# Kernel tuning notes

Measured on AMD Instinct MI355X. Metric: run time of the kernel, lower is better.

## Reference

```python
import jax, jax.numpy as jnp
import numpy as np

B_, S, D = 4, 1024, 1024
MULT, HEAD_DIM, M, K, CFAC = 4, 64, 16, 2, 1.25
H = MULT * D


def _layer_norm(x, g, b, eps=1e-5):
    mu = jnp.mean(x, axis=-1, keepdims=True)
    var = jnp.var(x, axis=-1, keepdims=True)
    return (x - mu) * jax.lax.rsqrt(var + eps) * g + b


def setup_inputs() -> dict:
    key = jax.random.key(0)
    ks = jax.random.split(key, 10)
    sc = 0.02
    return {
        "x": jax.random.normal(ks[0], (B_, S, D), jnp.float32),
        "ln1_g": jnp.ones((D,), jnp.float32), "ln1_b": jnp.zeros((D,), jnp.float32),
        "qkv_w": jax.random.normal(ks[1], (3 * D, D), jnp.float32) * sc,
        "qkv_b": jnp.zeros((3 * D,), jnp.float32),
        "attn_in_w": jax.random.normal(ks[2], (3 * D, D), jnp.float32) * sc,
        "attn_in_b": jnp.zeros((3 * D,), jnp.float32),
        "attn_out_w": jax.random.normal(ks[3], (D, D), jnp.float32) * sc,
        "attn_out_b": jnp.zeros((D,), jnp.float32),
        "ln2_g": jnp.ones((D,), jnp.float32), "ln2_b": jnp.zeros((D,), jnp.float32),
        "r_w1": jax.random.normal(ks[4], (H, D), jnp.float32) * sc,
        "r_b1": jnp.zeros((H,), jnp.float32),
        "r_w2": jax.random.normal(ks[5], (M, H), jnp.float32) * sc,
        "r_b2": jnp.zeros((M,), jnp.float32),
        "mlp1": jax.random.normal(ks[6], (M, D, H), jnp.float32) / np.float32(np.sqrt(D)),
        "mlp2": jax.random.normal(ks[7], (M, H, D), jnp.float32) / np.float32(np.sqrt(H)),
    }


def reference(x, ln1_g, ln1_b, qkv_w, qkv_b, attn_in_w, attn_in_b,
              attn_out_w, attn_out_b, ln2_g, ln2_b, r_w1, r_b1, r_w2, r_b2,
              mlp1, mlp2):
    b, s, d = x.shape
    nh, hd = d // HEAD_DIM, HEAD_DIM

    # ---- attention block ----
    resid = x
    xn = _layer_norm(x, ln1_g, ln1_b)
    qkv = xn @ qkv_w.T + qkv_b              # [b,s,3d]
    q0, k0, v0 = jnp.split(qkv, 3, axis=-1)
    # nn.MultiheadAttention applies its own in/out projections on top
    wq, wk, wv = jnp.split(attn_in_w, 3, axis=0)
    bq, bk, bv = jnp.split(attn_in_b, 3, axis=0)
    q = (q0 @ wq.T + bq).reshape(b, s, nh, hd).transpose(0, 2, 1, 3)
    k = (k0 @ wk.T + bk).reshape(b, s, nh, hd).transpose(0, 2, 1, 3)
    v = (v0 @ wv.T + bv).reshape(b, s, nh, hd).transpose(0, 2, 1, 3)
    scores = jnp.einsum('bhqd,bhkd->bhqk', q, k) / np.float32(np.sqrt(hd))
    causal = jnp.triu(jnp.full((s, s), -jnp.inf, jnp.float32), k=1)
    attn = jax.nn.softmax(scores + causal, axis=-1)
    ao = jnp.einsum('bhqk,bhkd->bhqd', attn, v).transpose(0, 2, 1, 3).reshape(b, s, d)
    x1 = resid + (ao @ attn_out_w.T + attn_out_b)

    # ---- MoE MLP block ----
    resid2 = x1
    xn2 = _layer_norm(x1, ln2_g, ln2_b)
    B = b * s
    cap = int(B * CFAC * K // M)
    xf = xn2.reshape(B, d)
    # router
    logits = jax.nn.gelu(xf @ r_w1.T + r_b1, approximate=False) @ r_w2.T + r_b2  # [B,M]
    vals, inds = jax.lax.top_k(logits, K)
    probs = jax.nn.softmax(vals, axis=-1).reshape(-1)     # [B*K]
    indsf = inds.reshape(-1)                              # [B*K]
    # cumsum-based position within each expert's capacity buffer
    one_hot = jax.nn.one_hot(indsf, M, dtype=jnp.int32)
    counts = jnp.cumsum(one_hot, axis=0)
    pos = counts[jnp.arange(B * K), indsf] - 1
    keep = pos < cap
    flat_idx = indsf * cap + pos
    safe_idx = jnp.where(keep, flat_idx, M * cap)         # OOB index -> dropped
    src = jnp.repeat(xf, K, axis=0)                       # [B*K, d]
    expert_in = jnp.zeros((M * cap, d), xf.dtype).at[safe_idx].set(src, mode='drop')
    expert_in = expert_in.reshape(M, cap, d)
    # grouped GEMM experts
    mid = jax.nn.gelu(jnp.einsum('mcd,mdh->mch', expert_in, mlp1), approximate=False)
    eout = jnp.einsum('mch,mhd->mcd', mid, mlp2).reshape(M * cap, d)
    # combine
    g = eout[jnp.where(keep, flat_idx, 0)] * (probs * keep)[:, None]
    token_idx = jnp.repeat(jnp.arange(B), K)
    combined = jax.ops.segment_sum(g, token_idx, num_segments=B)
    has_kept = jax.ops.segment_sum(keep.astype(jnp.int32), token_idx, num_segments=B) > 0
    moe_out = jnp.where(has_kept[:, None], combined, xf)
    out = resid2 + moe_out.reshape(b, s, d)
    return out, logits.reshape(b, s, M)
```

## Files before the change

kernel.cpp:

```cpp
#include <hip/hip_runtime.h>
#include <math.h>

#define NTOK   4096
#define DIM    1024
#define H3     3072
#define HMLP   4096
#define NEXP   16
#define CAP    640
#define HCHUNK 1024
#define LSCALE 2048.0f
#define INV_LSCALE (1.0f / 2048.0f)

typedef _Float16 half8 __attribute__((ext_vector_type(8)));
typedef __attribute__((ext_vector_type(4))) float floatx4;
typedef __attribute__((ext_vector_type(8))) ushort us8;

#define F_QKV_HI   ((size_t)0)
#define F_QKV_LO   ((size_t)6291456)
#define F_XN_HI    ((size_t)12582912)
#define F_XN_LO    ((size_t)14680064)
#define F_H1       ((size_t)0)
#define F_EOUT     ((size_t)0)
#define F_Q16_HI   ((size_t)16777216)
#define F_K16_HI   ((size_t)18874368)
#define F_V16_HI   ((size_t)20971520)
#define F_Q16_LO   ((size_t)23068672)
#define F_K16_LO   ((size_t)25165824)
#define F_V16_LO   ((size_t)27262976)
#define F_VT_HI    ((size_t)12582912)
#define F_VT_LO    ((size_t)14680064)
#define F_AO_HI    ((size_t)29360128)
#define F_AO_LO    ((size_t)31457280)
#define F_XF_HI    ((size_t)33554432)
#define F_XF_LO    ((size_t)35651584)
#define F_WQKV_HI  ((size_t)37748736)
#define F_WQKV_LO  ((size_t)39321600)
#define F_WAIN_HI  ((size_t)40894464)
#define F_WAIN_LO  ((size_t)42467328)
#define F_WAOUT_HI ((size_t)44040192)
#define F_WAOUT_LO ((size_t)44564480)
#define F_WR1_HI   ((size_t)45088768)
#define F_WR1_LO   ((size_t)47185920)
#define F_EXPIN    ((size_t)16777216)
#define F_MLP1T    ((size_t)22020096)
#define F_MID      ((size_t)30408704)
#define F_MLP2T    ((size_t)35651584)
#define F_X1       ((size_t)49283072)
#define F_XF       ((size_t)53477376)
#define F_PROBS    ((size_t)57671680)
#define F_INDS     ((size_t)57679872)
#define F_KEEP     ((size_t)57688064)
#define F_FLAT     ((size_t)57696256)

__device__ __forceinline__ ushort f2h(float f) {
    _Float16 h = (_Float16)f;
    union { _Float16 h; ushort u; } c; c.h = h; return c.u;
}
__device__ __forceinline__ float h2f(ushort u) {
    union { ushort u; _Float16 h; } c; c.u = u; return (float)c.h;
}
__device__ __forceinline__ float gelu_exact(float x) {
    return 0.5f * x * (1.0f + erff(x * 0.7071067811865475f));
}

__device__ __forceinline__ void gl16(const void* g, void* l) {
    __builtin_amdgcn_global_load_lds(
        (const __attribute__((address_space(1))) void*)g,
        (__attribute__((address_space(3))) void*)l, 16, 0, 0);
}

__global__ __launch_bounds__(256) void split_f32(const float* __restrict__ x,
                                                 ushort* __restrict__ hi,
                                                 ushort* __restrict__ lo, int n4) {
    int i = blockIdx.x * 256 + threadIdx.x;
    if (i >= n4) return;
    float4 v = ((const float4*)x)[i];
    float vv[4] = {v.x, v.y, v.z, v.w};
    ushort h[4], l[4];
#pragma unroll
    for (int e = 0; e < 4; e++) {
        h[e] = f2h(vv[e]);
        l[e] = f2h((vv[e] - h2f(h[e])) * LSCALE);
    }
    ((ushort4*)hi)[i] = make_ushort4(h[0], h[1], h[2], h[3]);
    ((ushort4*)lo)[i] = make_ushort4(l[0], l[1], l[2], l[3]);
}

__global__ __launch_bounds__(256) void ln_kernel(const float* __restrict__ x,
                                                 const float* __restrict__ g,
                                                 const float* __restrict__ b,
                                                 float* __restrict__ yf,
                                                 ushort* __restrict__ yhi,
                                                 ushort* __restrict__ ylo) {
    __shared__ float red0[4], red1[4], bc[2];
    const size_t t = blockIdx.x;
    const float* row = x + t * DIM;
    float v[4];
    float s = 0.f, s2 = 0.f;
#pragma unroll
    for (int i = 0; i < 4; i++) {
        float vv = row[threadIdx.x + i * 256];
        v[i] = vv; s += vv; s2 += vv * vv;
    }
#pragma unroll
    for (int off = 32; off > 0; off >>= 1) {
        s  += __shfl_down(s, off);
        s2 += __shfl_down(s2, off);
    }
    const int lane = threadIdx.x & 63, wid = threadIdx.x >> 6;
    if (lane == 0) { red0[wid] = s; red1[wid] = s2; }
    __syncthreads();
    if (threadIdx.x == 0) {
        float S = red0[0] + red0[1] + red0[2] + red0[3];
        float S2 = red1[0] + red1[1] + red1[2] + red1[3];
        float mean = S * (1.0f / DIM);
        float var = S2 * (1.0f / DIM) - mean * mean;
        bc[0] = mean; bc[1] = rsqrtf(var + 1e-5f);
    }
    __syncthreads();
    const float mean = bc[0], r = bc[1];
#pragma unroll
    for (int i = 0; i < 4; i++) {
        int idx = threadIdx.x + i * 256;
        float val = (v[i] - mean) * r * g[idx] + b[idx];
        size_t o = t * DIM + idx;
        if (yf) yf[o] = val;
        if (yhi) {
            ushort h = f2h(val);
            yhi[o] = h;
            if (ylo) ylo[o] = f2h((val - h2f(h)) * LSCALE);
        }
    }
}

template<bool SPLIT>
__global__ __launch_bounds__(256) void gemm_ht(
    const ushort* __restrict__ Ahi, const ushort* __restrict__ Alo, int lda, long long sA,
    const ushort* __restrict__ Bhi, const ushort* __restrict__ Blo, int ldb, long long sB,
    const float* __restrict__ bias, long long sBias,
    const float* __restrict__ resid, int ldr,
    float* __restrict__ outf, ushort* __restrict__ outhi, ushort* __restrict__ outlo,
    int ldc, long long sC, int Kdim, int act, int accum) {
    __shared__ ushort sAh[128][32];
    __shared__ ushort sBh[128][32];
    __shared__ ushort sAl[SPLIT ? 128 : 1][32];
    __shared__ ushort sBl[SPLIT ? 128 : 1][32];
    const int z = blockIdx.z;
    Ahi += (size_t)z * sA; Bhi += (size_t)z * sB;
    if constexpr (SPLIT) { Alo += (size_t)z * sA; Blo += (size_t)z * sB; }
    if (bias) bias += (size_t)z * sBias;
    if (outf) outf += (size_t)z * sC;
    if (outhi) outhi += (size_t)z * sC;
    if (outlo) outlo += (size_t)z * sC;

    const int tid = threadIdx.x;
    const int row0 = blockIdx.y * 128, col0 = blockIdx.x * 128;
    const int lane = tid & 63;
    const int m = lane & 15, half = lane >> 4;
    const int w = tid >> 6;
    const int ar0 = (w >> 1) * 64, bc0 = (w & 1) * 64;

    const int srow = w * 32 + (lane >> 2);
    const int ssw  = (((lane >> 3) & 3) ^ (lane & 3)) * 8;
    const int rsw8 = ((((m >> 1) & 3) ^ half)) * 8;

    floatx4 acc[4][4];
    floatx4 acc2[SPLIT ? 4 : 1][SPLIT ? 4 : 1];
#pragma unroll
    for (int i = 0; i < 4; i++)
#pragma unroll
        for (int j = 0; j < 4; j++) acc[i][j] = (floatx4){0.f, 0.f, 0.f, 0.f};
    if constexpr (SPLIT) {
#pragma unroll
        for (int i = 0; i < 4; i++)
#pragma unroll
            for (int j = 0; j < 4; j++) acc2[i][j] = (floatx4){0.f, 0.f, 0.f, 0.f};
    }

    for (int k0 = 0; k0 < Kdim; k0 += 32) {
        __syncthreads();
        {
            const ushort* gA = Ahi + (size_t)(row0 + srow) * lda + k0 + ssw;
            const ushort* gB = Bhi + (size_t)(col0 + srow) * ldb + k0 + ssw;
            gl16(gA,                      &sAh[w * 32][0]);
            gl16(gA + (size_t)16 * lda,   &sAh[w * 32 + 16][0]);
            gl16(gB,                      &sBh[w * 32][0]);
            gl16(gB + (size_t)16 * ldb,   &sBh[w * 32 + 16][0]);
            if constexpr (SPLIT) {
                const ushort* gAl = Alo + (size_t)(row0 + srow) * lda + k0 + ssw;
                const ushort* gBl = Blo + (size_t)(col0 + srow) * ldb + k0 + ssw;
                gl16(gAl,                    &sAl[w * 32][0]);
                gl16(gAl + (size_t)16 * lda, &sAl[w * 32 + 16][0]);
                gl16(gBl,                    &sBl[w * 32][0]);
                gl16(gBl + (size_t)16 * ldb, &sBl[w * 32 + 16][0]);
            }
        }
        __syncthreads();
        half8 fa[4], fb[4], fal[4], fbl[4];
#pragma unroll
        for (int i = 0; i < 4; i++) fa[i] = *(const half8*)&sAh[ar0 + i * 16 + m][rsw8];
#pragma unroll
        for (int j = 0; j < 4; j++) fb[j] = *(const half8*)&sBh[bc0 + j * 16 + m][rsw8];
        if constexpr (SPLIT) {
#pragma unroll
            for (int i = 0; i < 4; i++) fal[i] = *(const half8*)&sAl[ar0 + i * 16 + m][rsw8];
#pragma unroll
            for (int j = 0; j < 4; j++) fbl[j] = *(const half8*)&sBl[bc0 + j * 16 + m][rsw8];
        }
#pragma unroll
        for (int i = 0; i < 4; i++)
#pragma unroll
            for (int j = 0; j < 4; j++) {
                acc[i][j] = __builtin_amdgcn_mfma_f32_16x16x32_f16(fa[i], fb[j], acc[i][j], 0, 0, 0);
                if constexpr (SPLIT) {
                    acc2[i][j] = __builtin_amdgcn_mfma_f32_16x16x32_f16(fa[i], fbl[j], acc2[i][j], 0, 0, 0);
                    acc2[i][j] = __builtin_amdgcn_mfma_f32_16x16x32_f16(fal[i], fb[j], acc2[i][j], 0, 0, 0);
                }
            }
    }
#pragma unroll
    for (int i = 0; i < 4; i++) {
#pragma unroll
        for (int j = 0; j < 4; j++) {
            const int col = col0 + bc0 + j * 16 + m;
            const float bv = bias ? bias[col] : 0.f;
#pragma unroll
            for (int r = 0; r < 4; r++) {
                const int row = row0 + ar0 + i * 16 + half * 4 + r;
                float v = acc[i][j][r];
                if constexpr (SPLIT) v += acc2[i][j][r] * INV_LSCALE;
                v += bv;
                if (resid) v += resid[(size_t)row * ldr + col];
                if (accum) v += outf[(size_t)row * ldc + col];
                if (act) v = gelu_exact(v);
                const size_t o = (size_t)row * ldc + col;
                if (outf) outf[o] = v;
                if (outhi) {
                    ushort h = f2h(v);
                    outhi[o] = h;
                    if (outlo) outlo[o] = f2h((v - h2f(h)) * LSCALE);
                }
            }
        }
    }
}

__global__ __launch_bounds__(256) void transpose_h(const float* __restrict__ in, long long sIn, int ldin,
                                                   ushort* __restrict__ out, long long sOut, int ldout) {
    __shared__ float t[32][33];
    const int z = blockIdx.z;
    in += (size_t)z * sIn; out += (size_t)z * sOut;
    const int cx = threadIdx.x & 31, ry = threadIdx.x >> 5;
    const int r0 = blockIdx.y * 32, c0 = blockIdx.x * 32;
#pragma unroll
    for (int rr = 0; rr < 4; rr++)
        t[ry + rr * 8][cx] = in[(size_t)(r0 + ry + rr * 8) * ldin + c0 + cx];
    __syncthreads();
#pragma unroll
    for (int rr = 0; rr < 4; rr++)
        out[(size_t)(c0 + ry + rr * 8) * ldout + r0 + cx] = f2h(t[cx][ry + rr * 8]);
}

__global__ __launch_bounds__(256) void vtrans_kernel(const ushort* __restrict__ vhi,
                                                     const ushort* __restrict__ vlo,
                                                     ushort* __restrict__ vthi,
                                                     ushort* __restrict__ vtlo) {
    __shared__ ushort th[32][72], tl[32][72];
    const int bh = blockIdx.y, b = bh >> 4, h = bh & 15;
    const int s0 = blockIdx.x * 32;
    const int t = threadIdx.x;
    {
        const int s = t >> 3, d0 = (t & 7) * 8;
        const size_t src = ((size_t)(b * 1024 + s0 + s)) * 1024 + h * 64 + d0;
        *(uint4*)&th[s][d0] = *(const uint4*)&vhi[src];
        *(uint4*)&tl[s][d0] = *(const uint4*)&vlo[src];
    }
    __syncthreads();
    {
        const int d = t >> 2, soff = (t & 3) * 8;
        us8 rh, rl;
#pragma unroll
        for (int e = 0; e < 8; e++) { rh[e] = th[soff + e][d]; rl[e] = tl[soff + e][d]; }
        const size_t dst = (size_t)bh * 65536 + (size_t)d * 1024 + s0 + soff;
        *(us8*)&vthi[dst] = rh;
        *(us8*)&vtlo[dst] = rl;
    }
}

__global__ __launch_bounds__(256, 2) void attn_mfma(
        const ushort* __restrict__ qh_, const ushort* __restrict__ ql_,
        const ushort* __restrict__ kh_, const ushort* __restrict__ kl_,
        const ushort* __restrict__ vth_, const ushort* __restrict__ vtl_,
        ushort* __restrict__ ao_hi, ushort* __restrict__ ao_lo) {
    __shared__ ushort plds[4][2][2048];
    const int bh = blockIdx.y;
    const int b = bh >> 4;
    const int qt = 7 - blockIdx.x;
    const int tid = threadIdx.x;
    const int w = tid >> 6, lane = tid & 63;
    const int m = lane & 15, hq = lane >> 4;
    const int wrow = qt * 128 + w * 32;
    const size_t cbase = ((size_t)b * 1024) * 1024 + (size_t)(bh & 15) * 64;
    const size_t vtbase = (size_t)bh * 65536;

    half8 qfh[2][2], qfl[2][2];
#pragma unroll
    for (int i = 0; i < 2; i++)
#pragma unroll
        for (int kk = 0; kk < 2; kk++) {
            const size_t o = cbase + (size_t)(wrow + i * 16 + m) * 1024 + kk * 32 + hq * 8;
            qfh[i][kk] = *(const half8*)&qh_[o];
            qfl[i][kk] = *(const half8*)&ql_[o];
        }

    floatx4 accO[2][4], accO2[2][4];
#pragma unroll
    for (int i = 0; i < 2; i++)
#pragma unroll
        for (int d = 0; d < 4; d++) {
            accO[i][d] = (floatx4){0.f, 0.f, 0.f, 0.f};
            accO2[i][d] = (floatx4){0.f, 0.f, 0.f, 0.f};
        }
    float mx[2][4], ls[2][4];
#pragma unroll
    for (int i = 0; i < 2; i++)
#pragma unroll
        for (int r = 0; r < 4; r++) { mx[i][r] = -3.0e38f; ls[i][r] = 0.f; }

    const int ntiles = (wrow + 31) / 64 + 1;
    for (int t = 0; t < ntiles; t++) {
        const int j0 = t * 64;
        floatx4 accS[2][4], accS2[2][4];
#pragma unroll
        for (int i = 0; i < 2; i++)
#pragma unroll
            for (int jf = 0; jf < 4; jf++) {
                accS[i][jf] = (floatx4){0.f, 0.f, 0.f, 0.f};
                accS2[i][jf] = (floatx4){0.f, 0.f, 0.f, 0.f};
            }
#pragma unroll
        for (int kk = 0; kk < 2; kk++) {
            half8 kfh[4], kfl[4];
#pragma unroll
            for (int jf = 0; jf < 4; jf++) {
                const size_t o = cbase + (size_t)(j0 + jf * 16 + m) * 1024 + kk * 32 + hq * 8;
                kfh[jf] = *(const half8*)&kh_[o];
                kfl[jf] = *(const half8*)&kl_[o];
            }
#pragma unroll
            for (int i = 0; i < 2; i++)
#pragma unroll
                for (int jf = 0; jf < 4; jf++) {
                    accS[i][jf] = __builtin_amdgcn_mfma_f32_16x16x32_f16(qfh[i][kk], kfh[jf], accS[i][jf], 0, 0, 0);
                    accS2[i][jf] = __builtin_amdgcn_mfma_f32_16x16x32_f16(qfh[i][kk], kfl[jf], accS2[i][jf], 0, 0, 0);
                    accS2[i][jf] = __builtin_amdgcn_mfma_f32_16x16x32_f16(qfl[i][kk], kfh[jf], accS2[i][jf], 0, 0, 0);
                }
        }
        const bool diag = (j0 + 63 > wrow);
        float p[2][4][4];
#pragma unroll
        for (int i = 0; i < 2; i++)
#pragma unroll
            for (int jf = 0; jf < 4; jf++)
#pragma unroll
                for (int r = 0; r < 4; r++) {
                    float s = (accS[i][jf][r] + accS2[i][jf][r] * INV_LSCALE) * 0.125f;
                    if (diag && (j0 + jf * 16 + m > wrow + i * 16 + hq * 4 + r)) s = -3.0e38f;
                    p[i][jf][r] = s;
                }
#pragma unroll
        for (int i = 0; i < 2; i++)
#pragma unroll
            for (int r = 0; r < 4; r++) {
                float tm = fmaxf(fmaxf(p[i][0][r], p[i][1][r]), fmaxf(p[i][2][r], p[i][3][r]));
#pragma unroll
                for (int off = 8; off > 0; off >>= 1) tm = fmaxf(tm, __shfl_xor(tm, off));
                const float mn = fmaxf(mx[i][r], tm);
                const float c = __expf(mx[i][r] - mn);
                mx[i][r] = mn;
                float rs = 0.f;
#pragma unroll
                for (int jf = 0; jf < 4; jf++) {
                    const float e = __expf(p[i][jf][r] - mn);
                    p[i][jf][r] = e;
                    rs += e;
                }
#pragma unroll
                for (int off = 8; off > 0; off >>= 1) rs += __shfl_xor(rs, off);
                ls[i][r] = ls[i][r] * c + rs;
#pragma unroll
                for (int d = 0; d < 4; d++) { accO[i][d][r] *= c; accO2[i][d][r] *= c; }
            }
#pragma unroll
        for (int i = 0; i < 2; i++)
#pragma unroll
            for (int jf = 0; jf < 4; jf++)
#pragma unroll
                for (int r = 0; r < 4; r++) {
                    const int row = i * 16 + hq * 4 + r;
                    const int idx = row * 64 + ((jf * 16 + m) ^ ((row & 7) << 3));
                    const float pv = p[i][jf][r];
                    const ushort hh = f2h(pv);
                    plds[w][0][idx] = hh;
                    plds[w][1][idx] = f2h((pv - h2f(hh)) * LSCALE);
                }
#pragma unroll
        for (int kk = 0; kk < 2; kk++) {
            half8 pfh[2], pfl[2], vfh[4], vfl[4];
#pragma unroll
            for (int i = 0; i < 2; i++) {
                const int row = i * 16 + m;
                const int idx = row * 64 + ((kk * 32 + hq * 8) ^ ((row & 7) << 3));
                pfh[i] = *(const half8*)&plds[w][0][idx];
                pfl[i] = *(const half8*)&plds[w][1][idx];
            }
#pragma unroll
            for (int d = 0; d < 4; d++) {
                const size_t o = vtbase + (size_t)(d * 16 + m) * 1024 + j0 + kk * 32 + hq * 8;
                vfh[d] = *(const half8*)&vth_[o];
                vfl[d] = *(const half8*)&vtl_[o];
            }
#pragma unroll
            for (int i = 0; i < 2; i++)
#pragma unroll
                for (int d = 0; d < 4; d++) {
                    accO[i][d] = __builtin_amdgcn_mfma_f32_16x16x32_f16(pfh[i], vfh[d], accO[i][d], 0, 0, 0);
                    accO2[i][d] = __builtin_amdgcn_mfma_f32_16x16x32_f16(pfh[i], vfl[d], accO2[i][d], 0, 0, 0);
                    accO2[i][d] = __builtin_amdgcn_mfma_f32_16x16x32_f16(pfl[i], vfh[d], accO2[i][d], 0, 0, 0);
                }
        }
    }
#pragma unroll
    for (int i = 0; i < 2; i++)
#pragma unroll
        for (int r = 0; r < 4; r++) {
            const float inv = 1.f / ls[i][r];
            const size_t rb = cbase + (size_t)(wrow + i * 16 + hq * 4 + r) * 1024;
#pragma unroll
            for (int d = 0; d < 4; d++) {
                const float v = (accO[i][d][r] + accO2[i][d][r] * INV_LSCALE) * inv;
                const ushort hh = f2h(v);
                const size_t o = rb + d * 16 + m;
                ao_hi[o] = hh;
                ao_lo[o] = f2h((v - h2f(hh)) * LSCALE);
            }
        }
}

__global__ __launch_bounds__(256) void router2_kernel(const float* __restrict__ h1,
                                                      const float* __restrict__ w2,
                                                      const float* __restrict__ b2,
                                                      float* __restrict__ logits_out,
                                                      float* __restrict__ probs,
                                                      int* __restrict__ inds) {
    __shared__ float red[16][4];
    __shared__ float lg[16];
    const int t = blockIdx.x;
    const float* hrow = h1 + (size_t)t * HMLP;
    float acc[16];
#pragma unroll
    for (int m = 0; m < 16; m++) acc[m] = 0.f;
    for (int i = 0; i < 16; i++) {
        int kk = threadIdx.x + i * 256;
        float hv = hrow[kk];
#pragma unroll
        for (int m = 0; m < 16; m++) acc[m] = fmaf(hv, w2[m * HMLP + kk], acc[m]);
    }
#pragma unroll
    for (int m = 0; m < 16; m++)
#pragma unroll
        for (int off = 32; off > 0; off >>= 1) acc[m] += __shfl_down(acc[m], off);
    const int lane = threadIdx.x & 63, wid = threadIdx.x >> 6;
    if (lane == 0) {
#pragma unroll
        for (int m = 0; m < 16; m++) red[m][wid] = acc[m];
    }
    __syncthreads();
    if (threadIdx.x < 16) {
        float v = red[threadIdx.x][0] + red[threadIdx.x][1] + red[threadIdx.x][2] + red[threadIdx.x][3]
                  + b2[threadIdx.x];
        lg[threadIdx.x] = v;
        logits_out[(size_t)t * 16 + threadIdx.x] = v;
    }
    __syncthreads();
    if (threadIdx.x == 0) {
        int i0 = 0; float v0 = lg[0];
        for (int m = 1; m < 16; m++) if (lg[m] > v0) { v0 = lg[m]; i0 = m; }
        int i1 = -1; float v1 = -3.4e38f;
        for (int m = 0; m < 16; m++) if (m != i0 && lg[m] > v1) { v1 = lg[m]; i1 = m; }
        float e1 = expf(v1 - v0);
        float den = 1.f + e1;
        inds[2 * t] = i0; inds[2 * t + 1] = i1;
        probs[2 * t] = 1.f / den; probs[2 * t + 1] = e1 / den;
    }
}

__global__ __launch_bounds__(256) void scan_kernel(const int* __restrict__ inds,
                                                   int* __restrict__ keep,
                                                   int* __restrict__ flat) {
    __shared__ int counts[256][16];
    const int t = threadIdx.x;
#pragma unroll
    for (int e = 0; e < 16; e++) counts[t][e] = 0;
    const int base = t * 32;
    for (int i = 0; i < 32; i++) counts[t][inds[base + i]]++;
    __syncthreads();
    if (t < 16) {
        int run = 0;
        for (int c = 0; c < 256; c++) { int tmp = counts[c][t]; counts[c][t] = run; run += tmp; }
    }
    __syncthreads();
    for (int i = 0; i < 32; i++) {
        int e = inds[base + i];
        int p = counts[t][e]++;
        keep[base + i] = (p < CAP) ? 1 : 0;
        flat[base + i] = e * CAP + p;
    }
}

__global__ __launch_bounds__(256) void scatter_kernel(const float* __restrict__ xf,
                                                      const int* __restrict__ keep,
                                                      const int* __restrict__ flat,
                                                      ushort* __restrict__ expert_in) {
    const int e = blockIdx.x;
    if (!keep[e]) return;
    const int token = e >> 1;
    const float* src = xf + (size_t)token * DIM;
    ushort* dst = expert_in + (size_t)flat[e] * DIM;
#pragma unroll
    for (int i = 0; i < 4; i++) dst[threadIdx.x + i * 256] = f2h(src[threadIdx.x + i * 256]);
}

__global__ __launch_bounds__(256) void combine_kernel(const float* __restrict__ x1,
                                                      const float* __restrict__ xf,
                                                      const float* __restrict__ eout,
                                                      const float* __restrict__ probs,
                                                      const int* __restrict__ keep,
                                                      const int* __restrict__ flat,
                                                      float* __restrict__ out) {
    const int t = blockIdx.x;
    const int k0 = keep[2 * t], k1 = keep[2 * t + 1];
    const float p0 = probs[2 * t], p1 = probs[2 * t + 1];
    const size_t f0 = (size_t)flat[2 * t] * DIM, f1 = (size_t)flat[2 * t + 1] * DIM;
    const bool has = (k0 || k1);
    const size_t base = (size_t)t * DIM;
#pragma unroll
    for (int i = 0; i < 4; i++) {
        const int idx = threadIdx.x + i * 256;
        float mo;
        if (has) {
            mo = 0.f;
            if (k0) mo += p0 * eout[f0 + idx];
            if (k1) mo += p1 * eout[f1 + idx];
        } else {
            mo = xf[base + idx];
        }
        out[base + idx] = x1[base + idx] + mo;
    }
}

extern "C" void kernel_launch(void* const* d_in, const int* in_sizes, int n_in,
                              void* d_out, int out_size, void* d_ws, size_t ws_size,
                              hipStream_t stream) {
    const float* x          = (const float*)d_in[0];
    const float* ln1_g      = (const float*)d_in[1];
    const float* ln1_b      = (const float*)d_in[2];
    const float* qkv_w      = (const float*)d_in[3];
    const float* qkv_b      = (const float*)d_in[4];
    const float* attn_in_w  = (const float*)d_in[5];
    const float* attn_in_b  = (const float*)d_in[6];
    const float* attn_out_w = (const float*)d_in[7];
    const float* attn_out_b = (const float*)d_in[8];
    const float* ln2_g      = (const float*)d_in[9];
    const float* ln2_b      = (const float*)d_in[10];
    const float* r_w1       = (const float*)d_in[11];
    const float* r_b1       = (const float*)d_in[12];
    const float* r_w2       = (const float*)d_in[13];
    const float* r_b2       = (const float*)d_in[14];
    const float* mlp1       = (const float*)d_in[15];
    const float* mlp2       = (const float*)d_in[16];

    float* ws = (float*)d_ws;
    ushort* qkv_hi   = (ushort*)(ws + F_QKV_HI);
    ushort* qkv_lo   = (ushort*)(ws + F_QKV_LO);
    ushort* xn_hi    = (ushort*)(ws + F_XN_HI);
    ushort* xn_lo    = (ushort*)(ws + F_XN_LO);
    float*  h1       = ws + F_H1;
    float*  eout     = ws + F_EOUT;
    ushort* q_hi     = (ushort*)(ws + F_Q16_HI);
    ushort* q_lo     = (ushort*)(ws + F_Q16_LO);
    ushort* v_hi     = (ushort*)(ws + F_V16_HI);
    ushort* v_lo     = (ushort*)(ws + F_V16_LO);
    ushort* k_hi     = (ushort*)(ws + F_K16_HI);
    ushort* k_lo     = (ushort*)(ws + F_K16_LO);
    ushort* vt_hi    = (ushort*)(ws + F_VT_HI);
    ushort* vt_lo    = (ushort*)(ws + F_VT_LO);
    ushort* ao_hi    = (ushort*)(ws + F_AO_HI);
    ushort* ao_lo    = (ushort*)(ws + F_AO_LO);
    ushort* xf_hi    = (ushort*)(ws + F_XF_HI);
    ushort* xf_lo    = (ushort*)(ws + F_XF_LO);
    ushort* wqkv_hi  = (ushort*)(ws + F_WQKV_HI);
    ushort* wqkv_lo  = (ushort*)(ws + F_WQKV_LO);
    ushort* wain_hi  = (ushort*)(ws + F_WAIN_HI);
    ushort* wain_lo  = (ushort*)(ws + F_WAIN_LO);
    ushort* waout_hi = (ushort*)(ws + F_WAOUT_HI);
    ushort* waout_lo = (ushort*)(ws + F_WAOUT_LO);
    ushort* wr1_hi   = (ushort*)(ws + F_WR1_HI);
    ushort* wr1_lo   = (ushort*)(ws + F_WR1_LO);
    ushort* expert_in= (ushort*)(ws + F_EXPIN);
    ushort* mlp1t    = (ushort*)(ws + F_MLP1T);
    ushort* mid      = (ushort*)(ws + F_MID);
    ushort* mlp2t    = (ushort*)(ws + F_MLP2T);
    float*  x1       = ws + F_X1;
    float*  xf       = ws + F_XF;
    float*  probs    = ws + F_PROBS;
    int*    inds     = (int*)(ws + F_INDS);
    int*    keep     = (int*)(ws + F_KEEP);
    int*    flat     = (int*)(ws + F_FLAT);

    float* out        = (float*)d_out;
    float* logits_out = out + (size_t)NTOK * DIM;

    split_f32<<<(3145728 / 4 + 255) / 256, 256, 0, stream>>>(qkv_w, wqkv_hi, wqkv_lo, 3145728 / 4);
    split_f32<<<(3145728 / 4 + 255) / 256, 256, 0, stream>>>(attn_in_w, wain_hi, wain_lo, 3145728 / 4);
    split_f32<<<(1048576 / 4 + 255) / 256, 256, 0, stream>>>(attn_out_w, waout_hi, waout_lo, 1048576 / 4);
    split_f32<<<(4194304 / 4 + 255) / 256, 256, 0, stream>>>(r_w1, wr1_hi, wr1_lo, 4194304 / 4);

    ln_kernel<<<NTOK, 256, 0, stream>>>(x, ln1_g, ln1_b, nullptr, xn_hi, xn_lo);
    gemm_ht<true><<<dim3(H3 / 128, NTOK / 128, 1), 256, 0, stream>>>(
        xn_hi, xn_lo, DIM, 0, wqkv_hi, wqkv_lo, DIM, 0, qkv_b, 0,
        nullptr, 0, nullptr, qkv_hi, qkv_lo, H3, 0, DIM, 0, 0);
    gemm_ht<true><<<dim3(DIM / 128, NTOK / 128, 3), 256, 0, stream>>>(
        qkv_hi, qkv_lo, H3, 1024, wain_hi, wain_lo, DIM, 1048576, attn_in_b, 1024,
        nullptr, 0, nullptr, q_hi, q_lo, DIM, 4194304, DIM, 0, 0);
    vtrans_kernel<<<dim3(32, 64), 256, 0, stream>>>(v_hi, v_lo, vt_hi, vt_lo);
    attn_mfma<<<dim3(8, 64), 256, 0, stream>>>(q_hi, q_lo, k_hi, k_lo, vt_hi, vt_lo, ao_hi, ao_lo);
    gemm_ht<true><<<dim3(DIM / 128, NTOK / 128, 1), 256, 0, stream>>>(
        ao_hi, ao_lo, DIM, 0, waout_hi, waout_lo, DIM, 0, attn_out_b, 0,
        x, DIM, x1, nullptr, nullptr, DIM, 0, DIM, 0, 0);
    ln_kernel<<<NTOK, 256, 0, stream>>>(x1, ln2_g, ln2_b, xf, xf_hi, xf_lo);
    gemm_ht<true><<<dim3(HMLP / 128, NTOK / 128, 1), 256, 0, stream>>>(
        xf_hi, xf_lo, DIM, 0, wr1_hi, wr1_lo, DIM, 0, r_b1, 0,
        nullptr, 0, h1, nullptr, nullptr, HMLP, 0, DIM, 1, 0);
    router2_kernel<<<NTOK, 256, 0, stream>>>(h1, r_w2, r_b2, logits_out, probs, inds);
    scan_kernel<<<1, 256, 0, stream>>>(inds, keep, flat);
    scatter_kernel<<<NTOK * 2, 256, 0, stream>>>(xf, keep, flat, expert_in);
    for (int c = 0; c < HMLP / HCHUNK; c++) {
        transpose_h<<<dim3(32, 32, NEXP), 256, 0, stream>>>(
            mlp1 + (size_t)c * HCHUNK, (long long)DIM * HMLP, HMLP, mlp1t, 1048576, DIM);
        gemm_ht<false><<<dim3(HCHUNK / 128, CAP / 128, NEXP), 256, 0, stream>>>(
            expert_in, nullptr, DIM, 655360, mlp1t, nullptr, DIM, 1048576, nullptr, 0,
            nullptr, 0, nullptr, mid, nullptr, HCHUNK, 655360, DIM, 1, 0);
        transpose_h<<<dim3(32, 32, NEXP), 256, 0, stream>>>(
            mlp2 + (size_t)c * HCHUNK * DIM, (long long)HMLP * DIM, DIM, mlp2t, 1048576, HCHUNK);
        gemm_ht<false><<<dim3(DIM / 128, CAP / 128, NEXP), 256, 0, stream>>>(
            mid, nullptr, HCHUNK, 655360, mlp2t, nullptr, HCHUNK, 1048576, nullptr, 0,
            nullptr, 0, eout, nullptr, nullptr, DIM, 655360, HCHUNK, 0, c > 0);
    }
    combine_kernel<<<NTOK, 256, 0, stream>>>(x1, xf, eout, probs, keep, flat, out);
}
```

Measured before the change: 2.283 ms.

## Stage attention K/V tiles in shared memory via direct global-to-LDS loads

Attention K and V^T hi/lo tiles are now loaded once per block into swizzled LDS buffers using global-to-LDS loads, one wave per buffer. All four waves read them from LDS instead of each wave fetching the same tiles from global memory. The grid is also transposed so that heads vary fastest and the heaviest query tiles launch first. In exchange, every tile iteration adds two block barriers, waves past the causal limit still join the loads, and LDS use per block grows.

New measurement: 2.127 ms. 1.07x faster.

```diff
diff --git a/kernel.cpp b/kernel.cpp
--- a/kernel.cpp
+++ b/kernel.cpp
@@ -292,10 +292,11 @@
         const ushort* __restrict__ kh_, const ushort* __restrict__ kl_,
         const ushort* __restrict__ vth_, const ushort* __restrict__ vtl_,
         ushort* __restrict__ ao_hi, ushort* __restrict__ ao_lo) {
+    __shared__ ushort Ksh[64][64], Ksl[64][64], Vsh[64][64], Vsl[64][64];
     __shared__ ushort plds[4][2][2048];
-    const int bh = blockIdx.y;
+    const int bh = blockIdx.x;
     const int b = bh >> 4;
-    const int qt = 7 - blockIdx.x;
+    const int qt = 7 - blockIdx.y;
     const int tid = threadIdx.x;
     const int w = tid >> 6, lane = tid & 63;
     const int m = lane & 15, hq = lane >> 4;
@@ -303,6 +304,11 @@
     const size_t cbase = ((size_t)b * 1024) * 1024 + (size_t)(bh & 15) * 64;
     const size_t vtbase = (size_t)bh * 65536;
 
+    const int srr = lane >> 3;
+    const int scs = ((lane & 7) ^ (srr & 7)) * 8;
+    const int rs0 = ((hq ^ (m & 7)) & 7) * 8;
+    const int rs1 = (((4 + hq) ^ (m & 7)) & 7) * 8;
+
     half8 qfh[2][2], qfl[2][2];
 #pragma unroll
     for (int i = 0; i < 2; i++)
@@ -327,9 +333,34 @@
 #pragma unroll
         for (int r = 0; r < 4; r++) { mx[i][r] = -3.0e38f; ls[i][r] = 0.f; }
 
-    const int ntiles = (wrow + 31) / 64 + 1;
-    for (int t = 0; t < ntiles; t++) {
+    const int NT = 2 * qt + 2;
+    for (int t = 0; t < NT; t++) {
         const int j0 = t * 64;
+        __syncthreads();
+        if (w == 0) {
+            const ushort* g = kh_ + cbase + (size_t)(j0 + srr) * 1024 + scs;
+#pragma unroll
+            for (int dma = 0; dma < 8; dma++)
+                gl16(g + (size_t)dma * 8 * 1024, &Ksh[dma * 8][0]);
+        } else if (w == 1) {
+            const ushort* g = kl_ + cbase + (size_t)(j0 + srr) * 1024 + scs;
+#pragma unroll
+            for (int dma = 0; dma < 8; dma++)
+                gl16(g + (size_t)dma * 8 * 1024, &Ksl[dma * 8][0]);
+        } else if (w == 2) {
+            const ushort* g = vth_ + vtbase + (size_t)srr * 1024 + j0 + scs;
+#pragma unroll
+            for (int dma = 0; dma < 8; dma++)
+                gl16(g + (size_t)dma * 8 * 1024, &Vsh[dma * 8][0]);
+        } else {
+            const ushort* g = vtl_ + vtbase + (size_t)srr * 1024 + j0 + scs;
+#pragma unroll
+            for (int dma = 0; dma < 8; dma++)
+                gl16(g + (size_t)dma * 8 * 1024, &Vsl[dma * 8][0]);
+        }
+        __syncthreads();
+        if (j0 > wrow + 31) continue;
+
         floatx4 accS[2][4], accS2[2][4];
 #pragma unroll
         for (int i = 0; i < 2; i++)
@@ -340,12 +371,12 @@
             }
 #pragma unroll
         for (int kk = 0; kk < 2; kk++) {
+            const int rsw = kk ? rs1 : rs0;
             half8 kfh[4], kfl[4];
 #pragma unroll
             for (int jf = 0; jf < 4; jf++) {
-                const size_t o = cbase + (size_t)(j0 + jf * 16 + m) * 1024 + kk * 32 + hq * 8;
-                kfh[jf] = *(const half8*)&kh_[o];
-                kfl[jf] = *(const half8*)&kl_[o];
+                kfh[jf] = *(const half8*)&Ksh[jf * 16 + m][rsw];
+                kfl[jf] = *(const half8*)&Ksl[jf * 16 + m][rsw];
             }
 #pragma unroll
             for (int i = 0; i < 2; i++)
@@ -406,6 +437,7 @@
                 }
 #pragma unroll
         for (int kk = 0; kk < 2; kk++) {
+            const int rsw = kk ? rs1 : rs0;
             half8 pfh[2], pfl[2], vfh[4], vfl[4];
 #pragma unroll
             for (int i = 0; i < 2; i++) {
@@ -416,9 +448,8 @@
             }
 #pragma unroll
             for (int d = 0; d < 4; d++) {
-                const size_t o = vtbase + (size_t)(d * 16 + m) * 1024 + j0 + kk * 32 + hq * 8;
-                vfh[d] = *(const half8*)&vth_[o];
-                vfl[d] = *(const half8*)&vtl_[o];
+                vfh[d] = *(const half8*)&Vsh[d * 16 + m][rsw];
+                vfl[d] = *(const half8*)&Vsl[d * 16 + m][rsw];
             }
 #pragma unroll
             for (int i = 0; i < 2; i++)
@@ -634,7 +665,7 @@
         qkv_hi, qkv_lo, H3, 1024, wain_hi, wain_lo, DIM, 1048576, attn_in_b, 1024,
         nullptr, 0, nullptr, q_hi, q_lo, DIM, 4194304, DIM, 0, 0);
     vtrans_kernel<<<dim3(32, 64), 256, 0, stream>>>(v_hi, v_lo, vt_hi, vt_lo);
-    attn_mfma<<<dim3(8, 64), 256, 0, stream>>>(q_hi, q_lo, k_hi, k_lo, vt_hi, vt_lo, ao_hi, ao_lo);
+    attn_mfma<<<dim3(64, 8), 256, 0, stream>>>(q_hi, q_lo, k_hi, k_lo, vt_hi, vt_lo, ao_hi, ao_lo);
     gemm_ht<true><<<dim3(DIM / 128, NTOK / 128, 1), 256, 0, stream>>>(
         ao_hi, ao_lo, DIM, 0, waout_hi, waout_lo, DIM, 0, attn_out_b, 0,
         x, DIM, x1, nullptr, nullptr, DIM, 0, DIM, 0, 0);
```
